# Kernel tuning notes

Measured on AMD Instinct MI355X. Metric: run time of the kernel, lower is better.

## Reference

```python
import jax, jax.numpy as jnp
import numpy as np

# ---- constants (from init_kwargs / Box defaults) ----
B, K, T = 32768, 256, 10
C_LIGHT, F0, DF = 3.0e8, 1.0e10, 3.0e4
D_EL = C_LIGHT / (2.0 * F0)            # half-wavelength spacing
SPATIAL = F0 * D_EL / C_LIGHT          # = 0.5
RANGE_C = 2.0 * DF / C_LIGHT           # = 2e-4
THETA_MIN, THETA_MAX = -60.0, 60.0
R_MIN, R_MAX = 0.0, 2000.0
BETA = 2.0
STEP_CLIP = 0.1
INIT_ALPHA, INIT_LAMBDA = 0.01, 0.001
ALPHA_MIN, ALPHA_MAX = 1e-6, 0.2
LAM_MIN, LAM_MAX = 1e-6, 1.0
EPS = 1e-6


def _atanh(y):
    return jnp.arctanh(jnp.clip(y, -1.0 + EPS, 1.0 - EPS))


def map_theta_r_to_u(theta_deg, r_m):
    mid = 0.5 * (THETA_MIN + THETA_MAX)
    half = 0.5 * (THETA_MAX - THETA_MIN)
    y = (theta_deg - mid) / half
    s = jnp.clip((r_m - R_MIN) / (R_MAX - R_MIN), EPS, 1.0 - EPS)
    u_r = _atanh(2.0 * s - 1.0)          # tanh r_box inverse
    return jnp.stack([_atanh(y), u_r], axis=-1)  # (B,2)


def map_u_to_theta_r(u):
    mid = 0.5 * (THETA_MIN + THETA_MAX)
    half = 0.5 * (THETA_MAX - THETA_MIN)
    theta = mid + half * jnp.tanh(u[:, 0])
    s = 0.5 * (jnp.tanh(u[:, 1]) + 1.0)
    r = R_MIN + (R_MAX - R_MIN) * s
    return theta, r


def steering(theta_deg, r_m):
    # FDA steering: phase_k = 2*pi*k*(0.5*sin(theta) - 2*df*r/c)
    k = jnp.arange(K, dtype=jnp.float32)
    th = theta_deg * (jnp.pi / 180.0)
    phase = (2.0 * jnp.pi) * k[None, :] * (
        SPATIAL * jnp.sin(th)[:, None] - RANGE_C * r_m[:, None])  # (B,K)
    inv_sqrt_k = 1.0 / np.sqrt(K)
    return jnp.cos(phase) * inv_sqrt_k, jnp.sin(phase) * inv_sqrt_k


def loglike_logistic(theta_deg, r_m, z_re, z_im):
    # 1-bit logistic log-likelihood, summed over array elements -> (B,)
    a_re, a_im = steering(theta_deg, r_m)
    ll = jax.nn.log_sigmoid(BETA * z_re * a_re) + jax.nn.log_sigmoid(BETA * z_im * a_im)
    return jnp.sum(ll, axis=-1)


def setup_inputs() -> dict:
    key = jax.random.key(0)
    k1, k2, k3, k4 = jax.random.split(key, 4)
    z_real = jnp.sign(jax.random.normal(k1, (B, K), dtype=jnp.float32))
    z_imag = jnp.sign(jax.random.normal(k2, (B, K), dtype=jnp.float32))
    theta0 = jax.random.uniform(k3, (B,), jnp.float32, -55.0, 55.0)
    r0 = jax.random.uniform(k4, (B,), jnp.float32, 100.0, 1900.0)
    a_raw0 = float(np.log(np.expm1(INIT_ALPHA)))   # inverse softplus
    l_raw0 = float(np.log(np.expm1(INIT_LAMBDA)))
    return {
        "z_real": z_real, "z_imag": z_imag,
        "theta0_deg": theta0, "r0_m": r0,
        "alpha_theta_raw": jnp.full((T,), a_raw0, jnp.float32),
        "alpha_r_raw": jnp.full((T,), a_raw0, jnp.float32),
        "lambda_theta_raw": jnp.full((T,), l_raw0, jnp.float32),
        "lambda_r_raw": jnp.full((T,), l_raw0, jnp.float32),
    }


def reference(z_real, z_imag, theta0_deg, r0_m,
              alpha_theta_raw, alpha_r_raw, lambda_theta_raw, lambda_r_raw):
    alpha_th = jnp.clip(jax.nn.softplus(alpha_theta_raw), ALPHA_MIN, ALPHA_MAX)
    alpha_r = jnp.clip(jax.nn.softplus(alpha_r_raw), ALPHA_MIN, ALPHA_MAX)
    lam_th = jnp.clip(jax.nn.softplus(lambda_theta_raw), LAM_MIN, LAM_MAX)
    lam_r = jnp.clip(jax.nn.softplus(lambda_r_raw), LAM_MIN, LAM_MAX)

    u0 = map_theta_r_to_u(theta0_deg, r0_m)  # (B,2)

    def neg_obj_sum(u):
        th, r = map_u_to_theta_r(u)
        return -jnp.sum(loglike_logistic(th, r, z_real, z_imag))

    grad_fn = jax.grad(neg_obj_sum)

    def body(u, params):
        a_th, a_r, l_th, l_r = params
        # first-order unroll: gradient is a constant w.r.t. outer autodiff
        g = jax.lax.stop_gradient(grad_fn(u))
        g = jnp.where(jnp.isfinite(g), g, 0.0)
        g_th, g_r = g[:, 0], g[:, 1]
        a_th = jnp.where(jnp.isfinite(a_th), a_th, INIT_ALPHA)
        a_r = jnp.where(jnp.isfinite(a_r), a_r, INIT_ALPHA)
        l_th = jnp.where(jnp.isfinite(l_th), l_th, INIT_LAMBDA)
        l_r = jnp.where(jnp.isfinite(l_r), l_r, INIT_LAMBDA)
        den_th = jnp.maximum(jnp.nan_to_num(
            jnp.maximum(jnp.abs(g_th), 1e-6) + l_th, nan=1.0, posinf=1.0, neginf=1.0), 1e-6)
        den_r = jnp.maximum(jnp.nan_to_num(
            jnp.maximum(jnp.abs(g_r), 1e-6) + l_r, nan=1.0, posinf=1.0, neginf=1.0), 1e-6)
        step_u = jnp.stack([a_th * g_th / den_th, a_r * g_r / den_r], axis=-1)
        step_u = jnp.clip(jnp.nan_to_num(step_u, nan=0.0, posinf=0.0, neginf=0.0),
                          -STEP_CLIP, STEP_CLIP)
        return u - step_u, None

    uT, _ = jax.lax.scan(body, u0, (alpha_th, alpha_r, lam_th, lam_r))
    theta_T, r_T = map_u_to_theta_r(uT)
    return jnp.stack([theta_T, r_T], axis=-1)  # (B,2)
```

## Files before the change

### kernel.cpp

```cpp
#include <hip/hip_runtime.h>
#include <cstdint>

#define PI_F 3.14159265358979323846f

__device__ __forceinline__ float fract_(float x)  { return __builtin_amdgcn_fractf(x); }
__device__ __forceinline__ float sin2pi_(float r) { return __builtin_amdgcn_sinf(r); }
__device__ __forceinline__ float cos2pi_(float r) { return __builtin_amdgcn_cosf(r); }

extern "C" __global__ void pack_signs(const float* __restrict__ zr,
                                      const float* __restrict__ zi,
                                      uint32_t* __restrict__ pr,
                                      uint32_t* __restrict__ pim) {
    const int t = blockIdx.x * 256 + threadIdx.x;
    const float a = zr[t];
    const float b = zi[t];
    unsigned long long br = __ballot(a < 0.0f);
    unsigned long long bi = __ballot(b < 0.0f);
    if ((threadIdx.x & 31) == 0) {
        const int sh = threadIdx.x & 32;
        pr [t >> 5] = (uint32_t)(br >> sh);
        pim[t >> 5] = (uint32_t)(bi >> sh);
    }
}

extern "C" __global__ void __launch_bounds__(256)
refine(const float* __restrict__ th0, const float* __restrict__ r0,
       const float* __restrict__ a_th_raw, const float* __restrict__ a_r_raw,
       const float* __restrict__ l_th_raw, const float* __restrict__ l_r_raw,
       const uint32_t* __restrict__ pr, const uint32_t* __restrict__ pim,
       float* __restrict__ out) {
    const int lane = threadIdx.x & 63;
    const int w    = threadIdx.x >> 6;
    const int item = blockIdx.x * 64 + lane;

    __shared__ float red[4][64];

    const uint32_t br0 = pr [item * 8 + w * 2 + 0];
    const uint32_t br1 = pr [item * 8 + w * 2 + 1];
    const uint32_t bi0 = pim[item * 8 + w * 2 + 0];
    const uint32_t bi1 = pim[item * 8 + w * 2 + 1];

    float y = th0[item] * (1.0f / 60.0f);
    y = fminf(fmaxf(y, -1.0f + 1e-6f), 1.0f - 1e-6f);
    float u0 = atanhf(y);
    float sR = r0[item] * (1.0f / 2000.0f);
    sR = fminf(fmaxf(sR, 1e-6f), 1.0f - 1e-6f);
    float u1 = atanhf(2.0f * sR - 1.0f);

    const float w64 = (float)(w * 64);

    for (int t = 0; t < 10; ++t) {
        const float ath = fminf(fmaxf(log1pf(expf(a_th_raw[t])), 1e-6f), 0.2f);
        const float ar  = fminf(fmaxf(log1pf(expf(a_r_raw [t])), 1e-6f), 0.2f);
        const float lth = fminf(fmaxf(log1pf(expf(l_th_raw[t])), 1e-6f), 1.0f);
        const float lr  = fminf(fmaxf(log1pf(expf(l_r_raw [t])), 1e-6f), 1.0f);

        const float T0 = tanhf(u0), T1 = tanhf(u1);
        const float th_rad = (PI_F / 3.0f) * T0;
        const float sth = sinf(th_rad), cth = cosf(th_rad);
        const float r   = 1000.0f * (T1 + 1.0f);
        const float crev = 0.5f * sth - 2e-4f * r;

        const float d4 = fract_(4.0f * crev);
        const float C4 = cos2pi_(d4), S4 = sin2pi_(d4);

        float c[4], s[4], kf[4], acc[4];
        #pragma unroll
        for (int m = 0; m < 4; ++m) {
            const float k0 = w64 + (float)m;
            const float rv = fract_(k0 * crev);
            c[m] = cos2pi_(rv);
            s[m] = sin2pi_(rv);
            kf[m]  = k0;
            acc[m] = 0.0f;
        }

        #pragma unroll
        for (int j = 0; j < 16; ++j) {
            #pragma unroll
            for (int m = 0; m < 4; ++m) {
                const int kl = m + 4 * j;
                const uint32_t wr = (kl < 32) ? br0 : br1;
                const uint32_t wi = (kl < 32) ? bi0 : bi1;
                const int sh = 31 - (kl & 31);
                const uint32_t mre = (wr << sh) & 0x80000000u;
                const uint32_t mim = (wi << sh) & 0x80000000u;
                const float cs = c[m], ss = s[m];
                const float zc = __uint_as_float(__float_as_uint(cs) ^ mim);
                const float zs = __uint_as_float(__float_as_uint(ss) ^ mre);
                const float w0 = zc - zs;
                const float u2 = ss * ss;
                const float t2 = fmaf(-2.0f, u2, 1.0f);
                const float sc = ss * cs;
                const float v  = sc * t2;
                const float W  = fmaf(v, -(1.0f / 196608.0f), w0 * 0.0625f);
                acc[m] = fmaf(kf[m], W, acc[m]);
                kf[m] += 4.0f;
                const float tA = ss * S4;
                const float tB = cs * S4;
                c[m] = fmaf(cs, C4, -tA);
                s[m] = fmaf(ss, C4, tB);
            }
        }
        float S = (acc[0] + acc[1]) + (acc[2] + acc[3]);

        red[w][lane] = S;
        __syncthreads();
        S = (red[0][lane] + red[1][lane]) + (red[2][lane] + red[3][lane]);
        __syncthreads();

        const float g0 = -(PI_F * PI_F / 3.0f) * cth * (1.0f - T0 * T0) * S;
        const float g1 = 0.4f * PI_F * (1.0f - T1 * T1) * S;
        const float den0 = fmaxf(fabsf(g0), 1e-6f) + lth;
        const float den1 = fmaxf(fabsf(g1), 1e-6f) + lr;
        float st0 = ath * g0 / den0;
        float st1 = ar  * g1 / den1;
        st0 = fminf(fmaxf(st0, -0.1f), 0.1f);
        st1 = fminf(fmaxf(st1, -0.1f), 0.1f);
        u0 -= st0;
        u1 -= st1;
    }

    if (w == 0) {
        const float thT = 60.0f * tanhf(u0);
        const float rT  = 1000.0f * (tanhf(u1) + 1.0f);
        reinterpret_cast<float2*>(out)[item] = make_float2(thT, rT);
    }
}

extern "C" void kernel_launch(void* const* d_in, const int* in_sizes, int n_in,
                              void* d_out, int out_size, void* d_ws, size_t ws_size,
                              hipStream_t stream) {
    const float* zr   = (const float*)d_in[0];
    const float* zi   = (const float*)d_in[1];
    const float* th0  = (const float*)d_in[2];
    const float* r0   = (const float*)d_in[3];
    const float* athr = (const float*)d_in[4];
    const float* arr  = (const float*)d_in[5];
    const float* lthr = (const float*)d_in[6];
    const float* lrr  = (const float*)d_in[7];

    const int B = in_sizes[2];
    const int BK = in_sizes[0];

    uint32_t* pr  = (uint32_t*)d_ws;
    uint32_t* pim = pr + (size_t)B * 8;

    pack_signs<<<BK / 256, 256, 0, stream>>>(zr, zi, pr, pim);
    refine<<<B / 64, 256, 0, stream>>>(th0, r0, athr, arr, lthr, lrr, pr, pim,
                                       (float*)d_out);
}
```

Baseline: 155.1 us.

## Fuse sign packing into refine kernel and split work across eight waves

Merges the sign-packing kernel into the refinement kernel, so each block ballots its own z signs straight into shared memory and the packed workspace round trip plus the second launch go away. Blocks grow to 512 threads, with each wave handling two of the four phase chains instead of four, which gives more parallelism per item. Wave 0 alone computes the per-item steering scalars and the update step, and shares them through LDS. This adds an extra barrier per iteration and leaves the other waves idle during the serial scalar work.

```diff
diff --git a/kernel.cpp b/kernel.cpp
--- a/kernel.cpp
+++ b/kernel.cpp
@@ -7,85 +7,105 @@
 __device__ __forceinline__ float sin2pi_(float r) { return __builtin_amdgcn_sinf(r); }
 __device__ __forceinline__ float cos2pi_(float r) { return __builtin_amdgcn_cosf(r); }
 
-extern "C" __global__ void pack_signs(const float* __restrict__ zr,
-                                      const float* __restrict__ zi,
-                                      uint32_t* __restrict__ pr,
-                                      uint32_t* __restrict__ pim) {
-    const int t = blockIdx.x * 256 + threadIdx.x;
-    const float a = zr[t];
-    const float b = zi[t];
-    unsigned long long br = __ballot(a < 0.0f);
-    unsigned long long bi = __ballot(b < 0.0f);
-    if ((threadIdx.x & 31) == 0) {
-        const int sh = threadIdx.x & 32;
-        pr [t >> 5] = (uint32_t)(br >> sh);
-        pim[t >> 5] = (uint32_t)(bi >> sh);
+extern "C" __global__ void __launch_bounds__(512, 4)
+refine_fused(const float* __restrict__ zr, const float* __restrict__ zi,
+             const float* __restrict__ th0, const float* __restrict__ r0,
+             const float* __restrict__ a_th_raw, const float* __restrict__ a_r_raw,
+             const float* __restrict__ l_th_raw, const float* __restrict__ l_r_raw,
+             float* __restrict__ out) {
+    const int tid   = threadIdx.x;
+    const int lane  = tid & 63;
+    const int wv    = tid >> 6;
+    const int item0 = blockIdx.x * 64;
+
+    __shared__ uint32_t s_pr[64][9];
+    __shared__ uint32_t s_pi[64][9];
+    __shared__ float    s_b[3][64];
+    __shared__ float    s_red[8][64];
+
+    {
+        const int win  = wv & 3;
+        const int iofs = wv >> 2;
+        const size_t base = (size_t)item0 * 256 + (size_t)(wv * 64) + lane;
+        #pragma unroll 4
+        for (int p = 0; p < 32; ++p) {
+            const float a = zr[base + (size_t)p * 512];
+            const float b = zi[base + (size_t)p * 512];
+            const unsigned long long ba = __ballot(a < 0.0f);
+            const unsigned long long bb = __ballot(b < 0.0f);
+            if (lane == 0) {
+                const int it = 2 * p + iofs;
+                s_pr[it][2 * win]     = (uint32_t)ba;
+                s_pr[it][2 * win + 1] = (uint32_t)(ba >> 32);
+                s_pi[it][2 * win]     = (uint32_t)bb;
+                s_pi[it][2 * win + 1] = (uint32_t)(bb >> 32);
+            }
+        }
     }
-}
 
-extern "C" __global__ void __launch_bounds__(256)
-refine(const float* __restrict__ th0, const float* __restrict__ r0,
-       const float* __restrict__ a_th_raw, const float* __restrict__ a_r_raw,
-       const float* __restrict__ l_th_raw, const float* __restrict__ l_r_raw,
-       const uint32_t* __restrict__ pr, const uint32_t* __restrict__ pim,
-       float* __restrict__ out) {
-    const int lane = threadIdx.x & 63;
-    const int w    = threadIdx.x >> 6;
-    const int item = blockIdx.x * 64 + lane;
+    float u0 = 0.0f, u1 = 0.0f;
+    if (wv == 0) {
+        const int item = item0 + lane;
+        float y = th0[item] * (1.0f / 60.0f);
+        y = fminf(fmaxf(y, -1.0f + 1e-6f), 1.0f - 1e-6f);
+        u0 = atanhf(y);
+        float sR = r0[item] * (1.0f / 2000.0f);
+        sR = fminf(fmaxf(sR, 1e-6f), 1.0f - 1e-6f);
+        u1 = atanhf(2.0f * sR - 1.0f);
+    }
+    __syncthreads();
 
-    __shared__ float red[4][64];
+    const int w_ = wv >> 1;
+    const uint32_t br0 = s_pr[lane][2 * w_];
+    const uint32_t br1 = s_pr[lane][2 * w_ + 1];
+    const uint32_t bi0 = s_pi[lane][2 * w_];
+    const uint32_t bi1 = s_pi[lane][2 * w_ + 1];
 
-    const uint32_t br0 = pr [item * 8 + w * 2 + 0];
-    const uint32_t br1 = pr [item * 8 + w * 2 + 1];
-    const uint32_t bi0 = pim[item * 8 + w * 2 + 0];
-    const uint32_t bi1 = pim[item * 8 + w * 2 + 1];
+    const float w64 = (float)(64 * w_);
+    const int   mA  = 2 * (wv & 1);
 
-    float y = th0[item] * (1.0f / 60.0f);
-    y = fminf(fmaxf(y, -1.0f + 1e-6f), 1.0f - 1e-6f);
-    float u0 = atanhf(y);
-    float sR = r0[item] * (1.0f / 2000.0f);
-    sR = fminf(fmaxf(sR, 1e-6f), 1.0f - 1e-6f);
-    float u1 = atanhf(2.0f * sR - 1.0f);
-
-    const float w64 = (float)(w * 64);
+    float T0 = 0.0f, T1 = 0.0f, cth = 0.0f;
 
     for (int t = 0; t < 10; ++t) {
-        const float ath = fminf(fmaxf(log1pf(expf(a_th_raw[t])), 1e-6f), 0.2f);
-        const float ar  = fminf(fmaxf(log1pf(expf(a_r_raw [t])), 1e-6f), 0.2f);
-        const float lth = fminf(fmaxf(log1pf(expf(l_th_raw[t])), 1e-6f), 1.0f);
-        const float lr  = fminf(fmaxf(log1pf(expf(l_r_raw [t])), 1e-6f), 1.0f);
+        if (wv == 0) {
+            T0 = tanhf(u0);
+            T1 = tanhf(u1);
+            const float th_rad = (PI_F / 3.0f) * T0;
+            const float sth = sinf(th_rad);
+            cth = cosf(th_rad);
+            const float r    = 1000.0f * (T1 + 1.0f);
+            const float crev = 0.5f * sth - 2e-4f * r;
+            const float d4   = fract_(4.0f * crev);
+            s_b[0][lane] = crev;
+            s_b[1][lane] = cos2pi_(d4);
+            s_b[2][lane] = sin2pi_(d4);
+        }
+        __syncthreads();
+        const float crev = s_b[0][lane];
+        const float C4   = s_b[1][lane];
+        const float S4   = s_b[2][lane];
 
-        const float T0 = tanhf(u0), T1 = tanhf(u1);
-        const float th_rad = (PI_F / 3.0f) * T0;
-        const float sth = sinf(th_rad), cth = cosf(th_rad);
-        const float r   = 1000.0f * (T1 + 1.0f);
-        const float crev = 0.5f * sth - 2e-4f * r;
-
-        const float d4 = fract_(4.0f * crev);
-        const float C4 = cos2pi_(d4), S4 = sin2pi_(d4);
-
-        float c[4], s[4], kf[4], acc[4];
+        float c[2], s[2], kf[2], acc[2];
         #pragma unroll
-        for (int m = 0; m < 4; ++m) {
-            const float k0 = w64 + (float)m;
+        for (int mm = 0; mm < 2; ++mm) {
+            const float k0 = w64 + (float)(mA + mm);
             const float rv = fract_(k0 * crev);
-            c[m] = cos2pi_(rv);
-            s[m] = sin2pi_(rv);
-            kf[m]  = k0;
-            acc[m] = 0.0f;
+            c[mm]   = cos2pi_(rv);
+            s[mm]   = sin2pi_(rv);
+            kf[mm]  = k0;
+            acc[mm] = 0.0f;
         }
 
         #pragma unroll
         for (int j = 0; j < 16; ++j) {
             #pragma unroll
-            for (int m = 0; m < 4; ++m) {
-                const int kl = m + 4 * j;
-                const uint32_t wr = (kl < 32) ? br0 : br1;
-                const uint32_t wi = (kl < 32) ? bi0 : bi1;
-                const int sh = 31 - (kl & 31);
+            for (int mm = 0; mm < 2; ++mm) {
+                const uint32_t wr = (j < 8) ? br0 : br1;
+                const uint32_t wi = (j < 8) ? bi0 : bi1;
+                const int sh = 31 - ((mA + mm + 4 * j) & 31);
                 const uint32_t mre = (wr << sh) & 0x80000000u;
                 const uint32_t mim = (wi << sh) & 0x80000000u;
-                const float cs = c[m], ss = s[m];
+                const float cs = c[mm], ss = s[mm];
                 const float zc = __uint_as_float(__float_as_uint(cs) ^ mim);
                 const float zs = __uint_as_float(__float_as_uint(ss) ^ mre);
                 const float w0 = zc - zs;
@@ -93,38 +113,48 @@
                 const float t2 = fmaf(-2.0f, u2, 1.0f);
                 const float sc = ss * cs;
                 const float v  = sc * t2;
-                const float W  = fmaf(v, -(1.0f / 196608.0f), w0 * 0.0625f);
-                acc[m] = fmaf(kf[m], W, acc[m]);
-                kf[m] += 4.0f;
+                const float Wk = fmaf(v, -(1.0f / 196608.0f), w0 * 0.0625f);
+                acc[mm] = fmaf(kf[mm], Wk, acc[mm]);
+                kf[mm] += 4.0f;
                 const float tA = ss * S4;
                 const float tB = cs * S4;
-                c[m] = fmaf(cs, C4, -tA);
-                s[m] = fmaf(ss, C4, tB);
+                c[mm] = fmaf(cs, C4, -tA);
+                s[mm] = fmaf(ss, C4, tB);
             }
         }
-        float S = (acc[0] + acc[1]) + (acc[2] + acc[3]);
 
-        red[w][lane] = S;
-        __syncthreads();
-        S = (red[0][lane] + red[1][lane]) + (red[2][lane] + red[3][lane]);
+        s_red[wv][lane] = acc[0] + acc[1];
         __syncthreads();
 
-        const float g0 = -(PI_F * PI_F / 3.0f) * cth * (1.0f - T0 * T0) * S;
-        const float g1 = 0.4f * PI_F * (1.0f - T1 * T1) * S;
-        const float den0 = fmaxf(fabsf(g0), 1e-6f) + lth;
-        const float den1 = fmaxf(fabsf(g1), 1e-6f) + lr;
-        float st0 = ath * g0 / den0;
-        float st1 = ar  * g1 / den1;
-        st0 = fminf(fmaxf(st0, -0.1f), 0.1f);
-        st1 = fminf(fmaxf(st1, -0.1f), 0.1f);
-        u0 -= st0;
-        u1 -= st1;
+        if (wv == 0) {
+            const float S0 = s_red[0][lane] + s_red[1][lane];
+            const float S1 = s_red[2][lane] + s_red[3][lane];
+            const float S2 = s_red[4][lane] + s_red[5][lane];
+            const float S3 = s_red[6][lane] + s_red[7][lane];
+            const float S  = (S0 + S1) + (S2 + S3);
+
+            const float ath = fminf(fmaxf(log1pf(expf(a_th_raw[t])), 1e-6f), 0.2f);
+            const float ar  = fminf(fmaxf(log1pf(expf(a_r_raw [t])), 1e-6f), 0.2f);
+            const float lth = fminf(fmaxf(log1pf(expf(l_th_raw[t])), 1e-6f), 1.0f);
+            const float lr  = fminf(fmaxf(log1pf(expf(l_r_raw [t])), 1e-6f), 1.0f);
+
+            const float g0 = -(PI_F * PI_F / 3.0f) * cth * (1.0f - T0 * T0) * S;
+            const float g1 = 0.4f * PI_F * (1.0f - T1 * T1) * S;
+            const float den0 = fmaxf(fabsf(g0), 1e-6f) + lth;
+            const float den1 = fmaxf(fabsf(g1), 1e-6f) + lr;
+            float st0 = ath * g0 / den0;
+            float st1 = ar  * g1 / den1;
+            st0 = fminf(fmaxf(st0, -0.1f), 0.1f);
+            st1 = fminf(fmaxf(st1, -0.1f), 0.1f);
+            u0 -= st0;
+            u1 -= st1;
+        }
     }
 
-    if (w == 0) {
+    if (wv == 0) {
         const float thT = 60.0f * tanhf(u0);
         const float rT  = 1000.0f * (tanhf(u1) + 1.0f);
-        reinterpret_cast<float2*>(out)[item] = make_float2(thT, rT);
+        reinterpret_cast<float2*>(out)[item0 + lane] = make_float2(thT, rT);
     }
 }
 
@@ -141,12 +171,7 @@
     const float* lrr  = (const float*)d_in[7];
 
     const int B = in_sizes[2];
-    const int BK = in_sizes[0];
 
-    uint32_t* pr  = (uint32_t*)d_ws;
-    uint32_t* pim = pr + (size_t)B * 8;
-
-    pack_signs<<<BK / 256, 256, 0, stream>>>(zr, zi, pr, pim);
-    refine<<<B / 64, 256, 0, stream>>>(th0, r0, athr, arr, lthr, lrr, pr, pim,
-                                       (float*)d_out);
+    refine_fused<<<B / 64, 512, 0, stream>>>(zr, zi, th0, r0, athr, arr, lthr, lrr,
+                                             (float*)d_out);
 }
```

Measured after the change: 169.6 us. 9.3% more time.

## Vectorize sign packing, precompute softplus params in LDS, double-buffer reduction

Applied to the files above, without the earlier changes.

The sign-packing kernel now has each thread read 32 consecutive floats as float4 loads and build one 32-bit mask itself, replacing per-element ballots and launching 32x fewer threads. In the refine kernel the per-step softplus/clamp of the 40 schedule parameters is computed once by 40 threads into shared memory rather than by every thread each iteration. The cross-wave reduction buffer is double-buffered by iteration parity so the second barrier per step can be removed. Risks are less coalesced per-thread strided loads in pack_signs and the correctness of the single-barrier parity scheme.

```diff
diff --git a/kernel.cpp b/kernel.cpp
--- a/kernel.cpp
+++ b/kernel.cpp
@@ -7,20 +7,22 @@
 __device__ __forceinline__ float sin2pi_(float r) { return __builtin_amdgcn_sinf(r); }
 __device__ __forceinline__ float cos2pi_(float r) { return __builtin_amdgcn_cosf(r); }
 
-extern "C" __global__ void pack_signs(const float* __restrict__ zr,
-                                      const float* __restrict__ zi,
-                                      uint32_t* __restrict__ pr,
-                                      uint32_t* __restrict__ pim) {
+extern "C" __global__ void __launch_bounds__(256)
+pack_signs(const float4* __restrict__ zr, const float4* __restrict__ zi,
+           uint32_t* __restrict__ pr, uint32_t* __restrict__ pim) {
     const int t = blockIdx.x * 256 + threadIdx.x;
-    const float a = zr[t];
-    const float b = zi[t];
-    unsigned long long br = __ballot(a < 0.0f);
-    unsigned long long bi = __ballot(b < 0.0f);
-    if ((threadIdx.x & 31) == 0) {
-        const int sh = threadIdx.x & 32;
-        pr [t >> 5] = (uint32_t)(br >> sh);
-        pim[t >> 5] = (uint32_t)(bi >> sh);
+    uint32_t wr = 0u, wi = 0u;
+    #pragma unroll
+    for (int q = 0; q < 8; ++q) {
+        const float4 a = zr[t * 8 + q];
+        const float4 b = zi[t * 8 + q];
+        wr |= ((uint32_t)(a.x < 0.f) << (4 * q))     | ((uint32_t)(a.y < 0.f) << (4 * q + 1))
+            | ((uint32_t)(a.z < 0.f) << (4 * q + 2)) | ((uint32_t)(a.w < 0.f) << (4 * q + 3));
+        wi |= ((uint32_t)(b.x < 0.f) << (4 * q))     | ((uint32_t)(b.y < 0.f) << (4 * q + 1))
+            | ((uint32_t)(b.z < 0.f) << (4 * q + 2)) | ((uint32_t)(b.w < 0.f) << (4 * q + 3));
     }
+    pr[t] = wr;
+    pim[t] = wi;
 }
 
 extern "C" __global__ void __launch_bounds__(256)
@@ -33,7 +35,17 @@
     const int w    = threadIdx.x >> 6;
     const int item = blockIdx.x * 64 + lane;
 
-    __shared__ float red[4][64];
+    __shared__ float sp[4][10];
+    __shared__ float red[2][4][64];
+
+    if (threadIdx.x < 40) {
+        const int a = threadIdx.x / 10, i = threadIdx.x % 10;
+        const float* src = (a == 0) ? a_th_raw : (a == 1) ? a_r_raw
+                         : (a == 2) ? l_th_raw : l_r_raw;
+        const float v  = log1pf(expf(src[i]));
+        const float hi = (a < 2) ? 0.2f : 1.0f;
+        sp[a][i] = fminf(fmaxf(v, 1e-6f), hi);
+    }
 
     const uint32_t br0 = pr [item * 8 + w * 2 + 0];
     const uint32_t br1 = pr [item * 8 + w * 2 + 1];
@@ -49,11 +61,10 @@
 
     const float w64 = (float)(w * 64);
 
+    __syncthreads();
+
     for (int t = 0; t < 10; ++t) {
-        const float ath = fminf(fmaxf(log1pf(expf(a_th_raw[t])), 1e-6f), 0.2f);
-        const float ar  = fminf(fmaxf(log1pf(expf(a_r_raw [t])), 1e-6f), 0.2f);
-        const float lth = fminf(fmaxf(log1pf(expf(l_th_raw[t])), 1e-6f), 1.0f);
-        const float lr  = fminf(fmaxf(log1pf(expf(l_r_raw [t])), 1e-6f), 1.0f);
+        const float ath = sp[0][t], ar = sp[1][t], lth = sp[2][t], lr = sp[3][t];
 
         const float T0 = tanhf(u0), T1 = tanhf(u1);
         const float th_rad = (PI_F / 3.0f) * T0;
@@ -104,10 +115,10 @@
         }
         float S = (acc[0] + acc[1]) + (acc[2] + acc[3]);
 
-        red[w][lane] = S;
+        const int p = t & 1;
+        red[p][w][lane] = S;
         __syncthreads();
-        S = (red[0][lane] + red[1][lane]) + (red[2][lane] + red[3][lane]);
-        __syncthreads();
+        S = (red[p][0][lane] + red[p][1][lane]) + (red[p][2][lane] + red[p][3][lane]);
 
         const float g0 = -(PI_F * PI_F / 3.0f) * cth * (1.0f - T0 * T0) * S;
         const float g1 = 0.4f * PI_F * (1.0f - T1 * T1) * S;
@@ -140,13 +151,14 @@
     const float* lthr = (const float*)d_in[6];
     const float* lrr  = (const float*)d_in[7];
 
-    const int B = in_sizes[2];
+    const int B  = in_sizes[2];
     const int BK = in_sizes[0];
 
     uint32_t* pr  = (uint32_t*)d_ws;
     uint32_t* pim = pr + (size_t)B * 8;
 
-    pack_signs<<<BK / 256, 256, 0, stream>>>(zr, zi, pr, pim);
+    pack_signs<<<(BK / 32) / 256, 256, 0, stream>>>((const float4*)zr, (const float4*)zi,
+                                                    pr, pim);
     refine<<<B / 64, 256, 0, stream>>>(th0, r0, athr, arr, lthr, lrr, pr, pim,
                                        (float*)d_out);
 }
```

After: 139.1 us. 1.12x faster.
